# Optimization experiments

Measured on AMD Instinct MI355X. Metric: run time of the kernel, lower is better.

The kernel has to match this reference:

```python
import jax, jax.numpy as jnp
import numpy as np


def setup_inputs() -> dict:
    key = jax.random.key(0)
    k1, k2, k3 = jax.random.split(key, 3)
    B, C, H, W, K = 8, 256, 128, 128, 19
    feature = jax.random.normal(k1, (B, C, H, W), dtype=jnp.float32)
    map_ = jax.random.uniform(k2, (B, K, H, W), dtype=jnp.float32)
    # nn.Parameter, shape (1,1,1,1,K); original inits to zeros, use small randn
    # so the output is non-trivial for kernel correctness checking.
    gamma = jax.random.normal(k3, (1, 1, 1, 1, K), dtype=jnp.float32) * 0.1
    return {"feature": feature, "map": map_, "gamma": gamma}


def reference(feature, map, gamma):
    # Original: for each class k, att[b,c] = sum_hw feature[b,c,h,w]*map[b,k,h,w],
    # out_k = sigmoid(att)[...,None,None] * feature; result = feature + sum_k out_k*gamma[k].
    # Collapse per-class loop into one batched contraction + fused gate-reduce.
    att = jnp.einsum('bchw,bkhw->bck', feature, map)          # [B,C,K]
    scale = jnp.einsum('bck,k->bc', jax.nn.sigmoid(att), gamma.reshape(-1))  # [B,C]
    return feature + feature * scale[:, :, None, None]
```

## Files before the change

kernel.cpp:

```cpp
#include <hip/hip_runtime.h>
#include <math.h>

#define BB 8
#define CC 256
#define KK 19
#define HW 16384
#define HW4 4096

#define CHUNK4 32
#define NS (HW4 / CHUNK4)


typedef float f32x4 __attribute__((ext_vector_type(4)));

typedef const __attribute__((address_space(4))) f32x4* cvec4p;
#define CVEC4(p) ((cvec4p)(unsigned long long)(p))

#define FOR_K(OP) OP(0) OP(1) OP(2) OP(3) OP(4) OP(5) OP(6) OP(7) OP(8) OP(9) \
                  OP(10) OP(11) OP(12) OP(13) OP(14) OP(15) OP(16) OP(17) OP(18)

__global__ __launch_bounds__(256) void CGM_k1_contract(
    const float* __restrict__ feature,
    const float* __restrict__ map_,
    float* __restrict__ att,
    float* __restrict__ part)
{
    const int bI = blockIdx.x;
    const int s  = bI & (NS - 1);
    const int b  = bI >> 7;
    const int c  = threadIdx.x;

    const float* mw = map_ + (size_t)b * KK * HW + (size_t)s * (CHUNK4 * 4);
#define DECLM(K) cvec4p cm##K = CVEC4(mw + (size_t)(K) * HW);
    FOR_K(DECLM)
#undef DECLM

    float acc[KK];
#define ZERO(K) acc[K] = 0.f;
    FOR_K(ZERO)
#undef ZERO

    const float4* fb = (const float4*)feature
                     + ((size_t)b * CC + c) * HW4 + s * CHUNK4;

#pragma unroll 1
    for (int g = 0; g < 4; ++g) {
        float4 f[8];
#pragma unroll
        for (int u = 0; u < 8; ++u) f[u] = fb[g * 8 + u];
#pragma unroll
        for (int u = 0; u < 8; ++u) {
            const int jj = g * 8 + u;
            const float4 fv = f[u];
#define STEP(K) { const f32x4 m = cm##K[jj]; \
                  acc[K] += fv.x * m.x + fv.y * m.y + fv.z * m.z + fv.w * m.w; }
            FOR_K(STEP)
#undef STEP
        }
    }

    if (part) {
#define FIN(K) { part[((size_t)((K) * BB + b) * NS + s) * CC + c] = acc[K]; }
        FOR_K(FIN)
#undef FIN
    } else {
#define FIN(K) atomicAdd(&att[(size_t)(b * CC + c) * KK + (K)], acc[K]);
        FOR_K(FIN)
#undef FIN
    }
}

__global__ __launch_bounds__(256) void CGM_k1b_reduce(
    const float* __restrict__ part,
    float* __restrict__ att)
{
    const int bk = blockIdx.x;
    const int b  = bk / KK;
    const int k  = bk - b * KK;
    const int t  = threadIdx.x;
    const int q  = t & 63;
    const int sg = t >> 6;

    const float4* p4 = (const float4*)(part + (size_t)(k * BB + b) * NS * CC)
                     + (size_t)(sg * 32) * 64 + q;

    float4 a0 = {0.f, 0.f, 0.f, 0.f}, a1 = a0, a2 = a0, a3 = a0;
#pragma unroll 2
    for (int i = 0; i < 32; i += 4) {
        const float4 v0 = p4[(size_t)(i + 0) * 64];
        const float4 v1 = p4[(size_t)(i + 1) * 64];
        const float4 v2 = p4[(size_t)(i + 2) * 64];
        const float4 v3 = p4[(size_t)(i + 3) * 64];
        a0.x += v0.x; a0.y += v0.y; a0.z += v0.z; a0.w += v0.w;
        a1.x += v1.x; a1.y += v1.y; a1.z += v1.z; a1.w += v1.w;
        a2.x += v2.x; a2.y += v2.y; a2.z += v2.z; a2.w += v2.w;
        a3.x += v3.x; a3.y += v3.y; a3.z += v3.z; a3.w += v3.w;
    }
    float4 r;
    r.x = (a0.x + a1.x) + (a2.x + a3.x);
    r.y = (a0.y + a1.y) + (a2.y + a3.y);
    r.z = (a0.z + a1.z) + (a2.z + a3.z);
    r.w = (a0.w + a1.w) + (a2.w + a3.w);

    __shared__ float4 red[4][64];
    red[sg][q] = r;
    __syncthreads();
    if (t < 64) {
        const float4 u0 = red[0][q], u1 = red[1][q], u2 = red[2][q], u3 = red[3][q];
        float4 o;
        o.x = (u0.x + u1.x) + (u2.x + u3.x);
        o.y = (u0.y + u1.y) + (u2.y + u3.y);
        o.z = (u0.z + u1.z) + (u2.z + u3.z);
        o.w = (u0.w + u1.w) + (u2.w + u3.w);
        float* d = att + ((size_t)b * CC + 4 * q) * KK + k;
        d[0 * KK] = o.x;
        d[1 * KK] = o.y;
        d[2 * KK] = o.z;
        d[3 * KK] = o.w;
    }
}

#define S2 8
#define CT2 16
#define CHUNK24 (HW4 / S2)

__global__ __launch_bounds__(256) void CGM_k2_apply(
    const float* __restrict__ feature,
    const float* __restrict__ gamma,
    const float* __restrict__ att,
    float* __restrict__ out)
{
    const int bI = blockIdx.x;
    const int ct = bI & 15;
    const int s  = (bI >> 4) & (S2 - 1);
    const int b  = bI >> 7;
    const int t  = threadIdx.x;
    const int c0 = ct * CT2;

    __shared__ float sgk[CT2 * KK];
    __shared__ float scale[CT2];

    for (int idx = t; idx < CT2 * KK; idx += 256) {
        const int c = idx / KK;
        const int k = idx - c * KK;
        const float a = att[(size_t)(b * CC + c0 + c) * KK + k];
        const float sig = 1.f / (1.f + __expf(-a));
        sgk[idx] = sig * gamma[k];
    }
    __syncthreads();

    if (t < CT2) {
        float ssum = 0.f;
#define ADDK(K) ssum += sgk[t * KK + (K)];
        FOR_K(ADDK)
#undef ADDK
        scale[t] = 1.f + ssum;
    }
    __syncthreads();

    const float4* f4 = (const float4*)feature + (size_t)(b * CC + c0) * HW4;
    float4*       o4 = (float4*)out           + (size_t)(b * CC + c0) * HW4;
    const int ibase = s * CHUNK24;
#pragma unroll
    for (int c = 0; c < CT2; ++c) {
        const float sc = scale[c];
#pragma unroll
        for (int r = 0; r < CHUNK24 / 256; ++r) {
            const int i = ibase + r * 256 + t;
            const float4 f = f4[(size_t)c * HW4 + i];
            float4 o;
            o.x = f.x * sc;
            o.y = f.y * sc;
            o.z = f.z * sc;
            o.w = f.w * sc;
            o4[(size_t)c * HW4 + i] = o;
        }
    }
}

extern "C" void kernel_launch(void* const* d_in, const int* in_sizes, int n_in,
                              void* d_out, int out_size, void* d_ws, size_t ws_size,
                              hipStream_t stream) {
    const float* feature = (const float*)d_in[0];
    const float* map_    = (const float*)d_in[1];
    const float* gamma   = (const float*)d_in[2];
    float* out           = (float*)d_out;
    float* att           = (float*)d_ws;

    const size_t att_bytes  = (size_t)BB * CC * KK * sizeof(float);
    const size_t part_off   = (att_bytes + 255) & ~(size_t)255;
    const size_t part_bytes = (size_t)KK * BB * NS * CC * sizeof(float);
    const bool   split      = ws_size >= part_off + part_bytes;
    float* part = split ? (float*)((char*)d_ws + part_off) : nullptr;

    if (!split) {
        hipMemsetAsync(att, 0, att_bytes, stream);
    }

    const int grid1 = BB * NS;
    CGM_k1_contract<<<grid1, 256, 0, stream>>>(feature, map_, att, part);

    if (split) {
        CGM_k1b_reduce<<<BB * KK, 256, 0, stream>>>(part, att);
    }

    const int grid2 = BB * S2 * (CC / CT2);
    CGM_k2_apply<<<grid2, 256, 0, stream>>>(feature, gamma, att, out);
}
```

Before: 346.3 us.

## Stage feature tiles through LDS with async global_load_lds double buffering

The contraction kernel now has each wave cooperatively load a 64-channel by 8-float4 feature tile into LDS with global_load_lds. The layout is XOR-swizzled, the tile is double-buffered, and explicit vmcnt waits pipeline loads against the FMA work. Before, each thread streamed its own channel row directly from global memory. The spatial chunk per block doubles, which halves the grid size and the partial-sum count, and the reduce kernel is adjusted to match. This should coalesce the feature loads and overlap memory with compute. The cost is fewer blocks for parallelism and dependence on hand-placed wait counts.

Result: faster. 314.3 us (-9.2%).

```diff
diff --git a/kernel.cpp b/kernel.cpp
--- a/kernel.cpp
+++ b/kernel.cpp
@@ -7,17 +7,25 @@
 #define HW 16384
 #define HW4 4096
 
-#define CHUNK4 32
-#define NS (HW4 / CHUNK4)
+#define SCH4 64
+#define NS2 (HW4 / SCH4)
 
 
 typedef float f32x4 __attribute__((ext_vector_type(4)));
+
+#define AS1C(p) ((const __attribute__((address_space(1))) void*)(p))
+#define AS3(p)  ((__attribute__((address_space(3))) void*)(p))
 
 typedef const __attribute__((address_space(4))) f32x4* cvec4p;
 #define CVEC4(p) ((cvec4p)(unsigned long long)(p))
 
 #define FOR_K(OP) OP(0) OP(1) OP(2) OP(3) OP(4) OP(5) OP(6) OP(7) OP(8) OP(9) \
                   OP(10) OP(11) OP(12) OP(13) OP(14) OP(15) OP(16) OP(17) OP(18)
+
+#define WVM(N) do {                                                      \
+    asm volatile("s_waitcnt vmcnt(" #N ")" ::: "memory");                \
+    __builtin_amdgcn_sched_barrier(0);                                   \
+} while (0)
 
 __global__ __launch_bounds__(256) void CGM_k1_contract(
     const float* __restrict__ feature,
@@ -26,45 +34,72 @@
     float* __restrict__ part)
 {
     const int bI = blockIdx.x;
-    const int s  = bI & (NS - 1);
-    const int b  = bI >> 7;
-    const int c  = threadIdx.x;
-
-    const float* mw = map_ + (size_t)b * KK * HW + (size_t)s * (CHUNK4 * 4);
+    const int s  = bI & (NS2 - 1);
+    const int b  = bI >> 6;
+    const int t  = threadIdx.x;
+    const int l  = t & 63;
+    const int w  = t >> 6;
+
+    __shared__ float4 buf[4][2][512];
+
+    const float* mw = map_ + (size_t)b * KK * HW + (size_t)s * (SCH4 * 4);
 #define DECLM(K) cvec4p cm##K = CVEC4(mw + (size_t)(K) * HW);
     FOR_K(DECLM)
 #undef DECLM
+
+    const float4* fbase = (const float4*)feature
+                        + ((size_t)b * CC + w * 64) * HW4 + s * SCH4;
 
     float acc[KK];
 #define ZERO(K) acc[K] = 0.f;
     FOR_K(ZERO)
 #undef ZERO
 
-    const float4* fb = (const float4*)feature
-                     + ((size_t)b * CC + c) * HW4 + s * CHUNK4;
-
-#pragma unroll 1
-    for (int g = 0; g < 4; ++g) {
-        float4 f[8];
-#pragma unroll
-        for (int u = 0; u < 8; ++u) f[u] = fb[g * 8 + u];
-#pragma unroll
-        for (int u = 0; u < 8; ++u) {
-            const int jj = g * 8 + u;
-            const float4 fv = f[u];
-#define STEP(K) { const f32x4 m = cm##K[jj]; \
+#define STAGE(PP, JT) do {                                               \
+    __builtin_amdgcn_sched_barrier(0);                                   \
+    _Pragma("unroll")                                                    \
+    for (int q = 0; q < 8; ++q) {                                        \
+        const int slot = q * 64 + l;                                     \
+        const int row  = slot >> 3;                                      \
+        const int js   = slot & 7;                                       \
+        const float4* g = fbase + (size_t)row * HW4                      \
+                        + (JT) * 8 + (js ^ (row & 7));                   \
+        __builtin_amdgcn_global_load_lds(AS1C(g),                        \
+            AS3(&buf[w][PP][slot]), 16, 0, 0);                           \
+    }                                                                    \
+} while (0)
+
+#define STEP(K) { const f32x4 m = cm##K[jj];                             \
                   acc[K] += fv.x * m.x + fv.y * m.y + fv.z * m.z + fv.w * m.w; }
-            FOR_K(STEP)
+#define COMPUTE(PP, JT) do {                                             \
+    _Pragma("unroll")                                                    \
+    for (int j = 0; j < 8; ++j) {                                        \
+        const int jj = (JT) * 8 + j;                                     \
+        const float4 fv = buf[w][PP][l * 8 + (j ^ (l & 7))];             \
+        FOR_K(STEP)                                                      \
+    }                                                                    \
+} while (0)
+
+    STAGE(0, 0); STAGE(1, 1);
+    WVM(8); COMPUTE(0, 0); STAGE(0, 2);
+    WVM(8); COMPUTE(1, 1); STAGE(1, 3);
+    WVM(8); COMPUTE(0, 2); STAGE(0, 4);
+    WVM(8); COMPUTE(1, 3); STAGE(1, 5);
+    WVM(8); COMPUTE(0, 4); STAGE(0, 6);
+    WVM(8); COMPUTE(1, 5); STAGE(1, 7);
+    WVM(8); COMPUTE(0, 6);
+    WVM(0); COMPUTE(1, 7);
+
+#undef STAGE
+#undef COMPUTE
 #undef STEP
-        }
-    }
 
     if (part) {
-#define FIN(K) { part[((size_t)((K) * BB + b) * NS + s) * CC + c] = acc[K]; }
+#define FIN(K) { part[((size_t)((K) * BB + b) * NS2 + s) * CC + t] = acc[K]; }
         FOR_K(FIN)
 #undef FIN
     } else {
-#define FIN(K) atomicAdd(&att[(size_t)(b * CC + c) * KK + (K)], acc[K]);
+#define FIN(K) atomicAdd(&att[(size_t)(b * CC + t) * KK + (K)], acc[K]);
         FOR_K(FIN)
 #undef FIN
     }
@@ -81,12 +116,12 @@
     const int q  = t & 63;
     const int sg = t >> 6;
 
-    const float4* p4 = (const float4*)(part + (size_t)(k * BB + b) * NS * CC)
-                     + (size_t)(sg * 32) * 64 + q;
+    const float4* p4 = (const float4*)(part + (size_t)(k * BB + b) * NS2 * CC)
+                     + (size_t)(sg * 16) * 64 + q;
 
     float4 a0 = {0.f, 0.f, 0.f, 0.f}, a1 = a0, a2 = a0, a3 = a0;
-#pragma unroll 2
-    for (int i = 0; i < 32; i += 4) {
+#pragma unroll
+    for (int i = 0; i < 16; i += 4) {
         const float4 v0 = p4[(size_t)(i + 0) * 64];
         const float4 v1 = p4[(size_t)(i + 1) * 64];
         const float4 v2 = p4[(size_t)(i + 2) * 64];
@@ -189,7 +224,7 @@
 
     const size_t att_bytes  = (size_t)BB * CC * KK * sizeof(float);
     const size_t part_off   = (att_bytes + 255) & ~(size_t)255;
-    const size_t part_bytes = (size_t)KK * BB * NS * CC * sizeof(float);
+    const size_t part_bytes = (size_t)KK * BB * NS2 * CC * sizeof(float);
     const bool   split      = ws_size >= part_off + part_bytes;
     float* part = split ? (float*)((char*)d_ws + part_off) : nullptr;
 
@@ -197,7 +232,7 @@
         hipMemsetAsync(att, 0, att_bytes, stream);
     }
 
-    const int grid1 = BB * NS;
+    const int grid1 = BB * NS2;
     CGM_k1_contract<<<grid1, 256, 0, stream>>>(feature, map_, att, part);
 
     if (split) {
```

## Stage feature tiles in LDS via direct global-to-LDS loads, split classes across waves

Applied to the files above, without the earlier changes.

The contraction kernel now stages a 64-channel by 128-element feature tile into shared memory with global_load_lds, using an XOR swizzle to avoid bank conflicts. Each of the four waves handles a group of about five classes, reading map rows through wave-uniform scalar pointers, and the grid is four times larger with each block covering a quarter of the channels. This is meant to cut per-thread register pressure from 19 accumulators and raise occupancy and parallelism. The cost is more blocks, map data loaded once per channel quarter, and an extra barrier.

Result: faster. 289.0 us (-16.6%).

```diff
diff --git a/kernel.cpp b/kernel.cpp
--- a/kernel.cpp
+++ b/kernel.cpp
@@ -13,11 +13,18 @@
 
 typedef float f32x4 __attribute__((ext_vector_type(4)));
 
+#define AS1C(p) ((const __attribute__((address_space(1))) void*)(p))
+#define AS3(p)  ((__attribute__((address_space(3))) void*)(p))
+
 typedef const __attribute__((address_space(4))) f32x4* cvec4p;
 #define CVEC4(p) ((cvec4p)(unsigned long long)(p))
 
-#define FOR_K(OP) OP(0) OP(1) OP(2) OP(3) OP(4) OP(5) OP(6) OP(7) OP(8) OP(9) \
-                  OP(10) OP(11) OP(12) OP(13) OP(14) OP(15) OP(16) OP(17) OP(18)
+static __device__ __forceinline__ const float* uniform_ptr(const float* p) {
+    unsigned long long u = (unsigned long long)p;
+    unsigned lo = __builtin_amdgcn_readfirstlane((unsigned)u);
+    unsigned hi = __builtin_amdgcn_readfirstlane((unsigned)(u >> 32));
+    return (const float*)(((unsigned long long)hi << 32) | lo);
+}
 
 __global__ __launch_bounds__(256) void CGM_k1_contract(
     const float* __restrict__ feature,
@@ -26,47 +33,84 @@
     float* __restrict__ part)
 {
     const int bI = blockIdx.x;
-    const int s  = bI & (NS - 1);
-    const int b  = bI >> 7;
-    const int c  = threadIdx.x;
-
-    const float* mw = map_ + (size_t)b * KK * HW + (size_t)s * (CHUNK4 * 4);
-#define DECLM(K) cvec4p cm##K = CVEC4(mw + (size_t)(K) * HW);
-    FOR_K(DECLM)
-#undef DECLM
-
-    float acc[KK];
-#define ZERO(K) acc[K] = 0.f;
-    FOR_K(ZERO)
-#undef ZERO
-
-    const float4* fb = (const float4*)feature
-                     + ((size_t)b * CC + c) * HW4 + s * CHUNK4;
-
-#pragma unroll 1
-    for (int g = 0; g < 4; ++g) {
-        float4 f[8];
-#pragma unroll
-        for (int u = 0; u < 8; ++u) f[u] = fb[g * 8 + u];
-#pragma unroll
-        for (int u = 0; u < 8; ++u) {
-            const int jj = g * 8 + u;
-            const float4 fv = f[u];
-#define STEP(K) { const f32x4 m = cm##K[jj]; \
-                  acc[K] += fv.x * m.x + fv.y * m.y + fv.z * m.z + fv.w * m.w; }
-            FOR_K(STEP)
-#undef STEP
-        }
-    }
-
+    const int q4 = bI & 3;
+    const int s  = (bI >> 2) & (NS - 1);
+    const int b  = bI >> 9;
+    const int t  = threadIdx.x;
+    const int l  = t & 63;
+    const int w  = t >> 6;
+
+    __shared__ float4 tile[2048];
+
+    const int klo = w * 5;
+    const float* mw_raw = map_ + (size_t)b * KK * HW + (size_t)klo * HW
+                        + (size_t)s * (CHUNK4 * 4);
+    const size_t k4off = (size_t)((w == 3) ? 3 : 4) * HW;
+    const float* mw  = uniform_ptr(mw_raw);
+    const float* m4b = uniform_ptr(mw_raw + k4off);
+
+    cvec4p cm0 = CVEC4(mw);
+    cvec4p cm1 = CVEC4(mw + 1 * (size_t)HW);
+    cvec4p cm2 = CVEC4(mw + 2 * (size_t)HW);
+    cvec4p cm3 = CVEC4(mw + 3 * (size_t)HW);
+    cvec4p cm4 = CVEC4(m4b);
+
+    const float4* fbase = (const float4*)feature
+                        + ((size_t)b * CC + q4 * 64) * HW4 + s * CHUNK4;
+
+#pragma unroll
+    for (int q = 0; q < 8; ++q) {
+        const int row = 16 * w + 2 * q + (l >> 5);
+        const int u   = l & 31;
+        const int src = (u & 24) | ((u ^ row) & 7);
+        const float4* g = fbase + (size_t)row * HW4 + src;
+        __builtin_amdgcn_global_load_lds(AS1C(g),
+            AS3(&tile[row * 32 + u]), 16, 0, 0);
+    }
+
+    float A0 = 0.f, A1 = 0.f, A2 = 0.f, A3 = 0.f, A4 = 0.f;
+
+    __syncthreads();
+
+#pragma unroll
+    for (int jp = 0; jp < 16; ++jp) {
+        const int j0 = jp * 2;
+        const int j1 = jp * 2 + 1;
+        const f32x4 n00 = cm0[j0];
+        const f32x4 n01 = cm1[j0];
+        const f32x4 n02 = cm2[j0];
+        const f32x4 n03 = cm3[j0];
+        const f32x4 n04 = cm4[j0];
+        const f32x4 n10 = cm0[j1];
+        const f32x4 n11 = cm1[j1];
+        const f32x4 n12 = cm2[j1];
+        const f32x4 n13 = cm3[j1];
+        const f32x4 n14 = cm4[j1];
+        const float4 f0 = tile[l * 32 + ((j0 & 24) | ((j0 ^ l) & 7))];
+        const float4 f1 = tile[l * 32 + ((j1 & 24) | ((j1 ^ l) & 7))];
+        A0 += f0.x * n00.x + f0.y * n00.y + f0.z * n00.z + f0.w * n00.w;
+        A1 += f0.x * n01.x + f0.y * n01.y + f0.z * n01.z + f0.w * n01.w;
+        A2 += f0.x * n02.x + f0.y * n02.y + f0.z * n02.z + f0.w * n02.w;
+        A3 += f0.x * n03.x + f0.y * n03.y + f0.z * n03.z + f0.w * n03.w;
+        A4 += f0.x * n04.x + f0.y * n04.y + f0.z * n04.z + f0.w * n04.w;
+        A0 += f1.x * n10.x + f1.y * n10.y + f1.z * n10.z + f1.w * n10.w;
+        A1 += f1.x * n11.x + f1.y * n11.y + f1.z * n11.z + f1.w * n11.w;
+        A2 += f1.x * n12.x + f1.y * n12.y + f1.z * n12.z + f1.w * n12.w;
+        A3 += f1.x * n13.x + f1.y * n13.y + f1.z * n13.z + f1.w * n13.w;
+        A4 += f1.x * n14.x + f1.y * n14.y + f1.z * n14.z + f1.w * n14.w;
+    }
+
+    const int cbase = q4 * 64 + l;
     if (part) {
-#define FIN(K) { part[((size_t)((K) * BB + b) * NS + s) * CC + c] = acc[K]; }
-        FOR_K(FIN)
-#undef FIN
+#define STK(KI, AV) if (klo + (KI) < KK) {                               \
+        part[((size_t)((klo + (KI)) * BB + b) * NS + s) * CC + cbase] = AV; }
+        STK(0, A0) STK(1, A1) STK(2, A2) STK(3, A3) STK(4, A4)
+#undef STK
     } else {
-#define FIN(K) atomicAdd(&att[(size_t)(b * CC + c) * KK + (K)], acc[K]);
-        FOR_K(FIN)
-#undef FIN
+#define STK(KI, AV) if (klo + (KI) < KK) {                               \
+        atomicAdd(&att[(size_t)(b * CC + cbase) * KK + klo + (KI)], AV); }
+        STK(0, A0) STK(1, A1) STK(2, A2) STK(3, A3) STK(4, A4)
+#undef STK
     }
 }
 
@@ -124,6 +168,9 @@
 #define CT2 16
 #define CHUNK24 (HW4 / S2)
 
+#define FOR_K(OP) OP(0) OP(1) OP(2) OP(3) OP(4) OP(5) OP(6) OP(7) OP(8) OP(9) \
+                  OP(10) OP(11) OP(12) OP(13) OP(14) OP(15) OP(16) OP(17) OP(18)
+
 __global__ __launch_bounds__(256) void CGM_k2_apply(
     const float* __restrict__ feature,
     const float* __restrict__ gamma,
@@ -197,7 +244,7 @@
         hipMemsetAsync(att, 0, att_bytes, stream);
     }
 
-    const int grid1 = BB * NS;
+    const int grid1 = BB * NS * 4;
     CGM_k1_contract<<<grid1, 256, 0, stream>>>(feature, map_, att, part);
 
     if (split) {
```
